# Kernel optimization log

Measured on AMD Instinct MI355X. Metric: run time of the kernel, lower is better.

The kernel has to match this reference:

```python
import jax, jax.numpy as jnp
import numpy as np

NUM_USERS = 100000
NUM_ITEMS = 50000
N_NODES = NUM_USERS + NUM_ITEMS
D = 64
N_LAYERS = 3
E = 2000000
B = 1024
ALPHA_PREF = 1.0


def setup_inputs() -> dict:
    key = jax.random.key(0)
    k1, k2, k3, k4 = jax.random.split(key, 4)
    embed = jax.random.normal(k1, (N_NODES, D), dtype=jnp.float32) * 0.1
    edge_index = jax.random.randint(k2, (2, E), 0, N_NODES, dtype=jnp.int32)
    users = jax.random.randint(k3, (B,), 0, NUM_USERS, dtype=jnp.int32)
    items = jax.random.randint(k4, (B,), 0, NUM_ITEMS, dtype=jnp.int32)
    return {"embed": embed, "edge_index": edge_index, "users": users, "items": items}


def _lightgcn_propagate(x, row, col, norm):
    # message: norm * x[row] (x_j = source), aggregated (add) at col (target)
    msg = norm[:, None] * x[row]                      # [E, D]
    return jnp.zeros_like(x).at[col].add(msg)         # [N, D]


def reference(embed, edge_index, users, items):
    row, col = edge_index[0], edge_index[1]
    n = embed.shape[0]
    # degree normalization (depends only on edge_index; same every layer)
    deg = jnp.zeros((n,), jnp.float32).at[row].add(1.0)
    deg_inv = jnp.clip(deg, 1.0, None) ** -0.5
    norm = deg_inv[row] * deg_inv[col]                # [E]

    x = embed
    for _ in range(N_LAYERS):
        x = _lightgcn_propagate(x, row, col, norm)

    u_emb = x[users]                                  # [B, D]
    i_emb = x[items + NUM_USERS]                      # [B, D]

    # mask = (row == users[:,None]) flattened selection of col; edge e is
    # selected once per batch element b with users[b] == row[e] -> multiplicity
    cnt = jnp.zeros((n,), jnp.float32).at[users].add(1.0)
    mult = cnt[row]                                   # [E] selection multiplicity

    # PreferenceShapley surrogate: softmax over selected neighbor embeddings
    # of alpha_pref * <neigh_emb, mean(u_emb)>, flattened over the batch.
    context = u_emb.mean(0)                           # [D]
    neigh = x[col]                                    # [E, D]
    logits = ALPHA_PREF * (neigh @ context)           # [E]
    masked = jnp.where(mult > 0, logits, -jnp.inf)
    mx = jnp.max(masked)
    ew = mult * jnp.exp(logits - mx)                  # [E] weighted exp (0 where unselected)
    z = jnp.clip(ew.sum(), 1e-12, None)
    neigh_aggr = (ew[:, None] * neigh).sum(0) / z     # [D]

    score = (u_emb * i_emb).sum(-1) + u_emb @ neigh_aggr  # [B]
    return jax.nn.sigmoid(score)
```

## Files before the change

kernel.cpp:

```cpp
#include <hip/hip_runtime.h>
#include <float.h>
#include <math.h>

#define NUM_USERS 100000
#define NUM_ITEMS 50000
#define NNODES    150000
#define DIM       64
#define NEDGE     2000000
#define BATCH     1024
#define SEL_CAP   (1 << 18)
#define LOGIT_BLOCKS 512

#define SLICES   1024
#define EPS      1956
#define NBUK     293
#define BCAP     8192
#define SCAP     16

__device__ __forceinline__ float wave_sum64(float v) {
    #pragma unroll
    for (int off = 32; off > 0; off >>= 1) v += __shfl_xor(v, off, 64);
    return v;
}

__device__ __forceinline__ float bf2f(unsigned short s) {
    return __uint_as_float(((unsigned int)s) << 16);
}
__device__ __forceinline__ unsigned short f2bf(float f) {
    unsigned int u = __float_as_uint(f);
    return (unsigned short)((u + 0x7fffu + ((u >> 16) & 1u)) >> 16);
}


__global__ __launch_bounds__(512) void sort_kernel(
        const int* __restrict__ row, const int* __restrict__ col,
        const int* __restrict__ ucnt,
        int* __restrict__ gcurC, int* __restrict__ gcurR,
        unsigned int* __restrict__ midC, unsigned short* __restrict__ midR,
        int* __restrict__ n_sel, int* __restrict__ sel_col, float* __restrict__ sel_w) {
    __shared__ unsigned int hc[NBUK], hr[NBUK];
    __shared__ int posC[NBUK], posR[NBUK];
    __shared__ unsigned int   stC[NBUK * SCAP];
    __shared__ unsigned short stR[NBUK * SCAP];
    __shared__ int lcnt, lbase, novfC, novfR;
    __shared__ uint2 ovfC[64];
    __shared__ unsigned int ovfR[64];
    __shared__ int2 buf[256];
    int blk = blockIdx.x, t = threadIdx.x;
    for (int i = t; i < NBUK; i += 512) { hc[i] = 0; hr[i] = 0; }
    if (t == 0) { lcnt = 0; novfC = 0; novfR = 0; }
    __syncthreads();
    int e0 = blk * EPS;
    int e1 = e0 + EPS; if (e1 > NEDGE) e1 = NEDGE;
    for (int base = e0 + t * 4; base < e1; base += 2048) {
        if (base + 4 <= e1) {
            int4 r4 = *(const int4*)(row + base);
            int4 c4 = *(const int4*)(col + base);
            #pragma unroll
            for (int q = 0; q < 4; ++q) {
                int c = (q == 0) ? c4.x : (q == 1) ? c4.y : (q == 2) ? c4.z : c4.w;
                int r = (q == 0) ? r4.x : (q == 1) ? r4.y : (q == 2) ? r4.z : r4.w;
                int bc = c >> 9;
                unsigned int kc = atomicAdd(&hc[bc], 1u);
                unsigned int v = ((unsigned int)(c & 511) << 18) | (unsigned int)r;
                if (kc < SCAP) stC[bc * SCAP + kc] = v;
                else { int i = atomicAdd(&novfC, 1); if (i < 64) ovfC[i] = make_uint2((unsigned int)bc, v); }
                int br = r >> 9;
                unsigned int kr = atomicAdd(&hr[br], 1u);
                if (kr < SCAP) stR[br * SCAP + kr] = (unsigned short)(r & 511);
                else { int i = atomicAdd(&novfR, 1); if (i < 64) ovfR[i] = ((unsigned int)br << 9) | (unsigned int)(r & 511); }
                int u = ucnt[r];
                if (u > 0) { int i = atomicAdd(&lcnt, 1); if (i < 256) buf[i] = make_int2(c, u); }
            }
        } else {
            for (int e = base; e < e1; ++e) {
                int r = row[e], c = col[e];
                int bc = c >> 9;
                unsigned int kc = atomicAdd(&hc[bc], 1u);
                unsigned int v = ((unsigned int)(c & 511) << 18) | (unsigned int)r;
                if (kc < SCAP) stC[bc * SCAP + kc] = v;
                else { int i = atomicAdd(&novfC, 1); if (i < 64) ovfC[i] = make_uint2((unsigned int)bc, v); }
                int br = r >> 9;
                unsigned int kr = atomicAdd(&hr[br], 1u);
                if (kr < SCAP) stR[br * SCAP + kr] = (unsigned short)(r & 511);
                else { int i = atomicAdd(&novfR, 1); if (i < 64) ovfR[i] = ((unsigned int)br << 9) | (unsigned int)(r & 511); }
                int u = ucnt[r];
                if (u > 0) { int i = atomicAdd(&lcnt, 1); if (i < 256) buf[i] = make_int2(c, u); }
            }
        }
    }
    __syncthreads();
    if (t < NBUK) {
        int cc = (int)hc[t]; if (cc > SCAP) cc = SCAP;
        int cr = (int)hr[t]; if (cr > SCAP) cr = SCAP;
        posC[t] = atomicAdd(&gcurC[t], cc);
        posR[t] = atomicAdd(&gcurR[t], cr);
    }
    if (t == 0) {
        int c = lcnt; c = c < 256 ? c : 256;
        lbase = atomicAdd(n_sel, c);
    }
    __syncthreads();
    for (int j = t; j < NBUK * SCAP; j += 512) {
        int b = j >> 4, k = j & (SCAP - 1);
        int cc = (int)hc[b]; if (cc > SCAP) cc = SCAP;
        if (k < cc) {
            int d = posC[b] + k;
            if (d < BCAP) midC[(size_t)b * BCAP + d] = stC[j];
        }
        int cr = (int)hr[b]; if (cr > SCAP) cr = SCAP;
        if (k < cr) {
            int d = posR[b] + k;
            if (d < BCAP) midR[(size_t)b * BCAP + d] = stR[j];
        }
    }
    int nc = novfC; nc = nc < 64 ? nc : 64;
    for (int i = t; i < nc; i += 512) {
        int b = (int)ovfC[i].x;
        int d = atomicAdd(&gcurC[b], 1);
        if (d < BCAP) midC[(size_t)b * BCAP + d] = ovfC[i].y;
    }
    int nr = novfR; nr = nr < 64 ? nr : 64;
    for (int i = t; i < nr; i += 512) {
        unsigned int pv = ovfR[i];
        int b = (int)(pv >> 9);
        int d = atomicAdd(&gcurR[b], 1);
        if (d < BCAP) midR[(size_t)b * BCAP + d] = (unsigned short)(pv & 511u);
    }
    int c = lcnt; c = c < 256 ? c : 256;
    int b = lbase;
    for (int i = t; i < c; i += 512) {
        int o = b + i;
        if (o < SEL_CAP) { sel_col[o] = buf[i].x; sel_w[o] = (float)buf[i].y; }
    }
}


__global__ __launch_bounds__(1024) void bfinal_kernel(
        const unsigned int* __restrict__ midC, const int* __restrict__ gcurC,
        const unsigned short* __restrict__ midR, const int* __restrict__ gcurR,
        const float4* __restrict__ embed,
        int* __restrict__ rptr, int* __restrict__ rend, int* __restrict__ src_sorted,
        float* __restrict__ dinv, float* __restrict__ dinv2,
        uint2* __restrict__ y0) {
    __shared__ int cnt[512], sm[512], cur[512];
    __shared__ float dinvL[512];
    int b = blockIdx.x, t = threadIdx.x;
    int s0 = b * BCAP;
    int cc = gcurC[b]; if (cc > BCAP) cc = BCAP;
    int s1 = s0 + cc;
    if (t < 512) cnt[t] = 0;
    __syncthreads();
    for (int i = s0 + t; i < s1; i += 1024) atomicAdd(&cnt[midC[i] >> 18], 1);
    __syncthreads();
    if (t < 512) sm[t] = cnt[t];
    __syncthreads();
    for (int off = 1; off < 512; off <<= 1) {
        int v = 0;
        if (t < 512 && t >= off) v = sm[t - off];
        __syncthreads();
        if (t < 512) sm[t] += v;
        __syncthreads();
    }
    if (t < 512) {
        int excl = s0 + sm[t] - cnt[t];
        int n = b * 512 + t;
        if (n < NNODES) { rptr[n] = excl; rend[n] = s0 + sm[t]; }
        cur[t] = excl;
    }
    if (b == 0 && t < 16) y0[(size_t)NNODES * 16 + t] = make_uint2(0u, 0u);
    __syncthreads();
    for (int i = s0 + t; i < s1; i += 1024) {
        unsigned int v = midC[i];
        int dst = atomicAdd(&cur[v >> 18], 1);
        src_sorted[dst] = (int)(v & 0x3FFFFu);
    }
    __syncthreads();
    if (t < 512) cnt[t] = 0;
    __syncthreads();
    int r0 = b * BCAP;
    int rc = gcurR[b]; if (rc > BCAP) rc = BCAP;
    int r1 = r0 + rc;
    for (int i = r0 + t; i < r1; i += 1024) atomicAdd(&cnt[midR[i]], 1);
    __syncthreads();
    if (t < 512) {
        int n = b * 512 + t;
        if (n < NNODES) {
            float d = fmaxf((float)cnt[t], 1.0f);
            float di = rsqrtf(d);
            dinv[n] = di; dinv2[n] = 1.0f / d;
            dinvL[t] = di;
        }
    }
    __syncthreads();
    int nbase = b * 512;
    int nmax = NNODES - nbase; if (nmax > 512) nmax = 512;
    if (nmax < 0) nmax = 0;
    for (int i = t; i < nmax * 16; i += 1024) {
        int ln = i >> 4, slot = i & 15;
        float d = dinvL[ln];
        float4 v = embed[(size_t)(nbase + ln) * 16 + slot];
        unsigned int w0 = (unsigned int)f2bf(v.x * d) | ((unsigned int)f2bf(v.y * d) << 16);
        unsigned int w1 = (unsigned int)f2bf(v.z * d) | ((unsigned int)f2bf(v.w * d) << 16);
        y0[(size_t)(nbase + ln) * 16 + slot] = make_uint2(w0, w1);
    }
}


#define ACC8(V) do { \
    a0 += __uint_as_float((V).x << 16); a1 += __uint_as_float((V).x & 0xffff0000u); \
    a2 += __uint_as_float((V).y << 16); a3 += __uint_as_float((V).y & 0xffff0000u); \
    a4 += __uint_as_float((V).z << 16); a5 += __uint_as_float((V).z & 0xffff0000u); \
    a6 += __uint_as_float((V).w << 16); a7 += __uint_as_float((V).w & 0xffff0000u); \
} while (0)

__device__ __forceinline__ void prop_node(
        const uint4* __restrict__ x_in, uint4* __restrict__ x_out,
        const int* __restrict__ ptr, const int* __restrict__ rend,
        const int* __restrict__ src,
        const float* __restrict__ scale, int node, int sl) {
    int i = ptr[node], e = rend[node];
    float sc = scale[node];
    float a0 = 0.f, a1 = 0.f, a2 = 0.f, a3 = 0.f;
    float a4 = 0.f, a5 = 0.f, a6 = 0.f, a7 = 0.f;
    int p0, p1, p2, p3;
    if (i + 4 <= e) { p0 = src[i]; p1 = src[i + 1]; p2 = src[i + 2]; p3 = src[i + 3]; }
    while (i + 8 <= e) {
        uint4 w0 = x_in[p0 * 8 + sl];
        uint4 w1 = x_in[p1 * 8 + sl];
        uint4 w2 = x_in[p2 * 8 + sl];
        uint4 w3 = x_in[p3 * 8 + sl];
        p0 = src[i + 4]; p1 = src[i + 5]; p2 = src[i + 6]; p3 = src[i + 7];
        i += 4;
        ACC8(w0); ACC8(w1); ACC8(w2); ACC8(w3);
    }
    if (i + 4 <= e) {
        uint4 w0 = x_in[p0 * 8 + sl];
        uint4 w1 = x_in[p1 * 8 + sl];
        uint4 w2 = x_in[p2 * 8 + sl];
        uint4 w3 = x_in[p3 * 8 + sl];
        i += 4;
        ACC8(w0); ACC8(w1); ACC8(w2); ACC8(w3);
    }
    if (i < e) {
        int q0 = src[i];
        int q1 = (i + 1 < e) ? src[i + 1] : NNODES;
        int q2 = (i + 2 < e) ? src[i + 2] : NNODES;
        uint4 w0 = x_in[q0 * 8 + sl];
        uint4 w1 = x_in[q1 * 8 + sl];
        uint4 w2 = x_in[q2 * 8 + sl];
        ACC8(w0); ACC8(w1); ACC8(w2);
    }
    uint4 o;
    o.x = (unsigned int)f2bf(a0 * sc) | ((unsigned int)f2bf(a1 * sc) << 16);
    o.y = (unsigned int)f2bf(a2 * sc) | ((unsigned int)f2bf(a3 * sc) << 16);
    o.z = (unsigned int)f2bf(a4 * sc) | ((unsigned int)f2bf(a5 * sc) << 16);
    o.w = (unsigned int)f2bf(a6 * sc) | ((unsigned int)f2bf(a7 * sc) << 16);
    x_out[(size_t)node * 8 + sl] = o;
}

__global__ __launch_bounds__(256, 8) void prop_kernel(
        const uint4* __restrict__ x_in, uint4* __restrict__ x_out,
        const int* __restrict__ ptr, const int* __restrict__ rend,
        const int* __restrict__ src,
        const float* __restrict__ scale) {
    int gid  = blockIdx.x * blockDim.x + threadIdx.x;
    int node = gid >> 3;
    int sl   = gid & 7;
    if (node > NNODES) return;
    if (node == NNODES) {
        x_out[(size_t)node * 8 + sl] = make_uint4(0u, 0u, 0u, 0u);
        return;
    }
    prop_node(x_in, x_out, ptr, rend, src, scale, node, sl);
}

__global__ __launch_bounds__(256, 8) void prop_list_kernel(
        const uint4* __restrict__ x_in, uint4* __restrict__ x_out,
        const int* __restrict__ ptr, const int* __restrict__ rend,
        const int* __restrict__ src,
        const float* __restrict__ scale,
        const int* __restrict__ users, const int* __restrict__ items,
        const int* __restrict__ sel_col, const int* __restrict__ n_sel_p) {
    int n = *n_sel_p; if (n > SEL_CAP) n = SEL_CAP;
    int total = (2 * BATCH + n) * 8;
    int nth = gridDim.x * blockDim.x;
    for (int gid = blockIdx.x * blockDim.x + threadIdx.x; gid < total; gid += nth) {
        int li = gid >> 3;
        int sl = gid & 7;
        int node;
        if (li < BATCH) {
            node = users[li];
        } else if (li < 2 * BATCH) {
            node = items[li - BATCH] + NUM_USERS;
        } else {
            node = sel_col[li - 2 * BATCH];
        }
        prop_node(x_in, x_out, ptr, rend, src, scale, node, sl);
    }
}


__global__ void ucnt_kernel(const int* __restrict__ users, int* __restrict__ ucnt) {
    int b = blockIdx.x * blockDim.x + threadIdx.x;
    if (b < BATCH) atomicAdd(&ucnt[users[b]], 1);
}

__global__ __launch_bounds__(256) void ctx_part_kernel(
        const unsigned short* __restrict__ x, const int* __restrict__ users,
        float* __restrict__ ctx) {
    __shared__ float sm[256];
    int lane = threadIdx.x & 63, wl = threadIdx.x >> 6;
    int b0 = blockIdx.x * 16 + wl * 4;
    float acc = 0.0f;
    #pragma unroll
    for (int k = 0; k < 4; ++k)
        acc += bf2f(x[users[b0 + k] * DIM + lane]);
    sm[threadIdx.x] = acc;
    __syncthreads();
    if (wl == 0)
        atomicAdd(&ctx[lane], sm[lane] + sm[64 + lane] + sm[128 + lane] + sm[192 + lane]);
}

__global__ void softmax_kernel(const unsigned short* __restrict__ x,
                               const float* __restrict__ ctx,
                               const int* __restrict__ sel_col,
                               const float* __restrict__ sel_w,
                               const int* __restrict__ n_sel_p,
                               float* __restrict__ S, float* __restrict__ zp) {
    __shared__ float smS[4 * 64];
    __shared__ float smZ[4];
    int lane = threadIdx.x & 63, wl = threadIdx.x >> 6;
    int n = *n_sel_p; if (n > SEL_CAP) n = SEL_CAP;
    float c = ctx[lane] * (1.0f / BATCH);
    float accS = 0.0f, accZ = 0.0f;
    int stride = gridDim.x * 4;
    for (int idx = blockIdx.x * 4 + wl; idx < n; idx += stride) {
        int node = sel_col[idx];
        float xv = bf2f(x[node * DIM + lane]);
        float v = wave_sum64(xv * c);
        float w = sel_w[idx] * __expf(v);
        accS = fmaf(w, xv, accS);
        accZ += w;
    }
    smS[wl * 64 + lane] = accS;
    if (lane == 0) smZ[wl] = accZ;
    __syncthreads();
    if (wl == 0) {
        float s = smS[lane] + smS[64 + lane] + smS[128 + lane] + smS[192 + lane];
        atomicAdd(&S[lane], s);
    }
    if (threadIdx.x == 0) atomicAdd(zp, smZ[0] + smZ[1] + smZ[2] + smZ[3]);
}

__global__ void score_kernel(const unsigned short* __restrict__ x, const int* __restrict__ users,
                             const int* __restrict__ items, const float* __restrict__ S,
                             const float* __restrict__ zp, float* __restrict__ out) {
    int gid = blockIdx.x * blockDim.x + threadIdx.x;
    int b = gid >> 6, lane = gid & 63;
    if (b >= BATCH) return;
    float z = fmaxf(*zp, 1e-12f);
    float na = S[lane] / z;
    int u = users[b], it = items[b] + NUM_USERS;
    float v = bf2f(x[u * DIM + lane]) * (bf2f(x[it * DIM + lane]) + na);
    v = wave_sum64(v);
    if (lane == 0) out[b] = 1.0f / (1.0f + __expf(-v));
}


extern "C" void kernel_launch(void* const* d_in, const int* in_sizes, int n_in,
                              void* d_out, int out_size, void* d_ws, size_t ws_size,
                              hipStream_t stream) {
    const float* embed = (const float*)d_in[0];
    const int*   edge  = (const int*)d_in[1];
    const int*   row   = edge;
    const int*   col   = edge + NEDGE;
    const int*   users = (const int*)d_in[2];
    const int*   items = (const int*)d_in[3];
    float*       out   = (float*)d_out;
    char*        ws    = (char*)d_ws;

    size_t off = 0;
    auto A = [&](size_t bytes) { size_t o = off; off += (bytes + 255) & ~(size_t)255; return o; };
    size_t o_midC  = A((size_t)NBUK * BCAP * 4);
    size_t o_midR  = A((size_t)NBUK * BCAP * 2);
    size_t o_xa    = A((size_t)(NNODES + 1) * DIM * 2);
    size_t o_xb    = A((size_t)(NNODES + 1) * DIM * 2);
    size_t o_src   = A((size_t)NBUK * BCAP * 4);
    size_t o_selc  = A((size_t)SEL_CAP * 4);
    size_t o_selw  = A((size_t)SEL_CAP * 4);
    size_t o_zero  = off;
    size_t o_ucnt  = A((size_t)NNODES * 4);
    size_t o_gcurC = A((size_t)NBUK * 4);
    size_t o_gcurR = A((size_t)NBUK * 4);
    size_t o_misc  = A(1024);
    size_t zero_bytes = off - o_zero;
    size_t o_dinv  = A((size_t)NNODES * 4);
    size_t o_dinv2 = A((size_t)NNODES * 4);
    size_t o_rptr  = A((size_t)NNODES * 4);
    size_t o_rend  = A((size_t)NNODES * 4);

    unsigned int*   midC = (unsigned int*)(ws + o_midC);
    unsigned short* midR = (unsigned short*)(ws + o_midR);
    unsigned short* xa   = (unsigned short*)(ws + o_xa);
    unsigned short* xb   = (unsigned short*)(ws + o_xb);
    int*   srcS  = (int*)(ws + o_src);
    int*   selc  = (int*)(ws + o_selc);
    float* selw  = (float*)(ws + o_selw);
    int*   ucnt  = (int*)(ws + o_ucnt);
    int*   gcurC = (int*)(ws + o_gcurC);
    int*   gcurR = (int*)(ws + o_gcurR);
    int*   nsel  = (int*)(ws + o_misc);
    float* zp    = (float*)(ws + o_misc + 8);
    float* S     = (float*)(ws + o_misc + 256);
    float* ctx   = (float*)(ws + o_misc + 512);
    float* dinv  = (float*)(ws + o_dinv);
    float* dinv2 = (float*)(ws + o_dinv2);
    int*   rptr  = (int*)(ws + o_rptr);
    int*   rend  = (int*)(ws + o_rend);

    hipMemsetAsync(ws + o_zero, 0, zero_bytes, stream);

    ucnt_kernel<<<(BATCH + 255) / 256, 256, 0, stream>>>(users, ucnt);

    sort_kernel<<<SLICES, 512, 0, stream>>>(row, col, ucnt, gcurC, gcurR,
                                            midC, midR, nsel, selc, selw);
    bfinal_kernel<<<NBUK, 1024, 0, stream>>>(midC, gcurC, midR, gcurR,
                                             (const float4*)embed, rptr, rend, srcS,
                                             dinv, dinv2, (uint2*)xa);

    int prop_blocks = ((NNODES + 1) * 8 + 255) / 256;
    prop_kernel<<<prop_blocks, 256, 0, stream>>>((const uint4*)xa, (uint4*)xb, rptr, rend, srcS, dinv2);
    prop_kernel<<<prop_blocks, 256, 0, stream>>>((const uint4*)xb, (uint4*)xa, rptr, rend, srcS, dinv2);
    prop_list_kernel<<<1024, 256, 0, stream>>>((const uint4*)xa, (uint4*)xb,
                                               rptr, rend, srcS, dinv,
                                               users, items, selc, nsel);

    ctx_part_kernel<<<64, 256, 0, stream>>>(xb, users, ctx);
    softmax_kernel<<<LOGIT_BLOCKS, 256, 0, stream>>>(xb, ctx, selc, selw, nsel, S, zp);

    score_kernel<<<(BATCH * 64 + 255) / 256, 256, 0, stream>>>(xb, users, items, S, zp, out);
}
```

Baseline: 256.4 us.

## Replace global atomic bucket cursors with fixed per-slice slots and global overflow list

The sort kernel now writes each slice's per-bucket staged edges into a fixed slot region indexed by slice, and records per-slice counts as bytes, instead of reserving space with global atomics on per-bucket cursors. Overflow entries go to a larger global list that the bucket-finalize kernel scans. This removes contended global atomics and the serialising cursor dependency in the sort kernel. In exchange the finalize kernel must scan a sparse padded layout of 16K slots per bucket, plus the whole overflow list in every block, which costs more reads.

```diff
diff --git a/kernel.cpp b/kernel.cpp
--- a/kernel.cpp
+++ b/kernel.cpp
@@ -16,6 +16,7 @@
 #define NBUK     293
 #define BCAP     8192
 #define SCAP     16
+#define OVF_CAP  4096
 
 __device__ __forceinline__ float wave_sum64(float v) {
     #pragma unroll
@@ -35,20 +36,19 @@
 __global__ __launch_bounds__(512) void sort_kernel(
         const int* __restrict__ row, const int* __restrict__ col,
         const int* __restrict__ ucnt,
-        int* __restrict__ gcurC, int* __restrict__ gcurR,
-        unsigned int* __restrict__ midC, unsigned short* __restrict__ midR,
+        unsigned char* __restrict__ cntC8, unsigned char* __restrict__ cntR8,
+        unsigned int* __restrict__ midC2, unsigned short* __restrict__ midR2,
+        uint2* __restrict__ ovfC, unsigned int* __restrict__ ovfR,
+        int* __restrict__ novfC_g, int* __restrict__ novfR_g,
         int* __restrict__ n_sel, int* __restrict__ sel_col, float* __restrict__ sel_w) {
     __shared__ unsigned int hc[NBUK], hr[NBUK];
-    __shared__ int posC[NBUK], posR[NBUK];
     __shared__ unsigned int   stC[NBUK * SCAP];
     __shared__ unsigned short stR[NBUK * SCAP];
-    __shared__ int lcnt, lbase, novfC, novfR;
-    __shared__ uint2 ovfC[64];
-    __shared__ unsigned int ovfR[64];
+    __shared__ int lcnt, lbase;
     __shared__ int2 buf[256];
     int blk = blockIdx.x, t = threadIdx.x;
     for (int i = t; i < NBUK; i += 512) { hc[i] = 0; hr[i] = 0; }
-    if (t == 0) { lcnt = 0; novfC = 0; novfR = 0; }
+    if (t == 0) lcnt = 0;
     __syncthreads();
     int e0 = blk * EPS;
     int e1 = e0 + EPS; if (e1 > NEDGE) e1 = NEDGE;
@@ -64,11 +64,11 @@
                 unsigned int kc = atomicAdd(&hc[bc], 1u);
                 unsigned int v = ((unsigned int)(c & 511) << 18) | (unsigned int)r;
                 if (kc < SCAP) stC[bc * SCAP + kc] = v;
-                else { int i = atomicAdd(&novfC, 1); if (i < 64) ovfC[i] = make_uint2((unsigned int)bc, v); }
+                else { int i = atomicAdd(novfC_g, 1); if (i < OVF_CAP) ovfC[i] = make_uint2((unsigned int)bc, v); }
                 int br = r >> 9;
                 unsigned int kr = atomicAdd(&hr[br], 1u);
                 if (kr < SCAP) stR[br * SCAP + kr] = (unsigned short)(r & 511);
-                else { int i = atomicAdd(&novfR, 1); if (i < 64) ovfR[i] = ((unsigned int)br << 9) | (unsigned int)(r & 511); }
+                else { int i = atomicAdd(novfR_g, 1); if (i < OVF_CAP) ovfR[i] = ((unsigned int)br << 9) | (unsigned int)(r & 511); }
                 int u = ucnt[r];
                 if (u > 0) { int i = atomicAdd(&lcnt, 1); if (i < 256) buf[i] = make_int2(c, u); }
             }
@@ -79,54 +79,37 @@
                 unsigned int kc = atomicAdd(&hc[bc], 1u);
                 unsigned int v = ((unsigned int)(c & 511) << 18) | (unsigned int)r;
                 if (kc < SCAP) stC[bc * SCAP + kc] = v;
-                else { int i = atomicAdd(&novfC, 1); if (i < 64) ovfC[i] = make_uint2((unsigned int)bc, v); }
+                else { int i = atomicAdd(novfC_g, 1); if (i < OVF_CAP) ovfC[i] = make_uint2((unsigned int)bc, v); }
                 int br = r >> 9;
                 unsigned int kr = atomicAdd(&hr[br], 1u);
                 if (kr < SCAP) stR[br * SCAP + kr] = (unsigned short)(r & 511);
-                else { int i = atomicAdd(&novfR, 1); if (i < 64) ovfR[i] = ((unsigned int)br << 9) | (unsigned int)(r & 511); }
+                else { int i = atomicAdd(novfR_g, 1); if (i < OVF_CAP) ovfR[i] = ((unsigned int)br << 9) | (unsigned int)(r & 511); }
                 int u = ucnt[r];
                 if (u > 0) { int i = atomicAdd(&lcnt, 1); if (i < 256) buf[i] = make_int2(c, u); }
             }
         }
     }
     __syncthreads();
+    for (int j = t; j < NBUK * SCAP; j += 512) {
+        int b = j >> 4, k = j & (SCAP - 1);
+        unsigned int cc = hc[b]; if (cc > SCAP) cc = SCAP;
+        if ((unsigned int)k < cc)
+            midC2[(size_t)b * (SLICES * SCAP) + blk * SCAP + k] = stC[j];
+        unsigned int cr = hr[b]; if (cr > SCAP) cr = SCAP;
+        if ((unsigned int)k < cr)
+            midR2[(size_t)b * (SLICES * SCAP) + blk * SCAP + k] = stR[j];
+    }
     if (t < NBUK) {
-        int cc = (int)hc[t]; if (cc > SCAP) cc = SCAP;
-        int cr = (int)hr[t]; if (cr > SCAP) cr = SCAP;
-        posC[t] = atomicAdd(&gcurC[t], cc);
-        posR[t] = atomicAdd(&gcurR[t], cr);
+        unsigned int cc = hc[t]; if (cc > SCAP) cc = SCAP;
+        unsigned int cr = hr[t]; if (cr > SCAP) cr = SCAP;
+        cntC8[(size_t)blk * NBUK + t] = (unsigned char)cc;
+        cntR8[(size_t)blk * NBUK + t] = (unsigned char)cr;
     }
     if (t == 0) {
         int c = lcnt; c = c < 256 ? c : 256;
         lbase = atomicAdd(n_sel, c);
     }
     __syncthreads();
-    for (int j = t; j < NBUK * SCAP; j += 512) {
-        int b = j >> 4, k = j & (SCAP - 1);
-        int cc = (int)hc[b]; if (cc > SCAP) cc = SCAP;
-        if (k < cc) {
-            int d = posC[b] + k;
-            if (d < BCAP) midC[(size_t)b * BCAP + d] = stC[j];
-        }
-        int cr = (int)hr[b]; if (cr > SCAP) cr = SCAP;
-        if (k < cr) {
-            int d = posR[b] + k;
-            if (d < BCAP) midR[(size_t)b * BCAP + d] = stR[j];
-        }
-    }
-    int nc = novfC; nc = nc < 64 ? nc : 64;
-    for (int i = t; i < nc; i += 512) {
-        int b = (int)ovfC[i].x;
-        int d = atomicAdd(&gcurC[b], 1);
-        if (d < BCAP) midC[(size_t)b * BCAP + d] = ovfC[i].y;
-    }
-    int nr = novfR; nr = nr < 64 ? nr : 64;
-    for (int i = t; i < nr; i += 512) {
-        unsigned int pv = ovfR[i];
-        int b = (int)(pv >> 9);
-        int d = atomicAdd(&gcurR[b], 1);
-        if (d < BCAP) midR[(size_t)b * BCAP + d] = (unsigned short)(pv & 511u);
-    }
     int c = lcnt; c = c < 256 ? c : 256;
     int b = lbase;
     for (int i = t; i < c; i += 512) {
@@ -137,21 +120,32 @@
 
 
 __global__ __launch_bounds__(1024) void bfinal_kernel(
-        const unsigned int* __restrict__ midC, const int* __restrict__ gcurC,
-        const unsigned short* __restrict__ midR, const int* __restrict__ gcurR,
+        const unsigned int* __restrict__ midC2, const unsigned char* __restrict__ cntC8,
+        const unsigned short* __restrict__ midR2, const unsigned char* __restrict__ cntR8,
+        const uint2* __restrict__ ovfC, const unsigned int* __restrict__ ovfR,
+        const int* __restrict__ novfC_g, const int* __restrict__ novfR_g,
         const float4* __restrict__ embed,
         int* __restrict__ rptr, int* __restrict__ rend, int* __restrict__ src_sorted,
         float* __restrict__ dinv, float* __restrict__ dinv2,
         uint2* __restrict__ y0) {
     __shared__ int cnt[512], sm[512], cur[512];
+    __shared__ unsigned char lcC[SLICES], lcR[SLICES];
     __shared__ float dinvL[512];
     int b = blockIdx.x, t = threadIdx.x;
-    int s0 = b * BCAP;
-    int cc = gcurC[b]; if (cc > BCAP) cc = BCAP;
-    int s1 = s0 + cc;
+    if (t < SLICES) {
+        lcC[t] = cntC8[(size_t)t * NBUK + b];
+        lcR[t] = cntR8[(size_t)t * NBUK + b];
+    }
     if (t < 512) cnt[t] = 0;
     __syncthreads();
-    for (int i = s0 + t; i < s1; i += 1024) atomicAdd(&cnt[midC[i] >> 18], 1);
+    size_t cbase = (size_t)b * (SLICES * SCAP);
+    for (int j = t; j < SLICES * SCAP; j += 1024) {
+        if ((unsigned int)(j & (SCAP - 1)) < (unsigned int)lcC[j >> 4])
+            atomicAdd(&cnt[midC2[cbase + j] >> 18], 1);
+    }
+    int noC = *novfC_g; if (noC > OVF_CAP) noC = OVF_CAP;
+    for (int i = t; i < noC; i += 1024)
+        if ((int)ovfC[i].x == b) atomicAdd(&cnt[ovfC[i].y >> 18], 1);
     __syncthreads();
     if (t < 512) sm[t] = cnt[t];
     __syncthreads();
@@ -162,6 +156,7 @@
         if (t < 512) sm[t] += v;
         __syncthreads();
     }
+    int s0 = b * BCAP;
     if (t < 512) {
         int excl = s0 + sm[t] - cnt[t];
         int n = b * 512 + t;
@@ -170,18 +165,31 @@
     }
     if (b == 0 && t < 16) y0[(size_t)NNODES * 16 + t] = make_uint2(0u, 0u);
     __syncthreads();
-    for (int i = s0 + t; i < s1; i += 1024) {
-        unsigned int v = midC[i];
-        int dst = atomicAdd(&cur[v >> 18], 1);
-        src_sorted[dst] = (int)(v & 0x3FFFFu);
-    }
+    for (int j = t; j < SLICES * SCAP; j += 1024) {
+        if ((unsigned int)(j & (SCAP - 1)) < (unsigned int)lcC[j >> 4]) {
+            unsigned int v = midC2[cbase + j];
+            int dst = atomicAdd(&cur[v >> 18], 1);
+            src_sorted[dst] = (int)(v & 0x3FFFFu);
+        }
+    }
+    for (int i = t; i < noC; i += 1024)
+        if ((int)ovfC[i].x == b) {
+            unsigned int v = ovfC[i].y;
+            int dst = atomicAdd(&cur[v >> 18], 1);
+            src_sorted[dst] = (int)(v & 0x3FFFFu);
+        }
     __syncthreads();
     if (t < 512) cnt[t] = 0;
     __syncthreads();
-    int r0 = b * BCAP;
-    int rc = gcurR[b]; if (rc > BCAP) rc = BCAP;
-    int r1 = r0 + rc;
-    for (int i = r0 + t; i < r1; i += 1024) atomicAdd(&cnt[midR[i]], 1);
+    for (int j = t; j < SLICES * SCAP; j += 1024) {
+        if ((unsigned int)(j & (SCAP - 1)) < (unsigned int)lcR[j >> 4])
+            atomicAdd(&cnt[midR2[cbase + j]], 1);
+    }
+    int noR = *novfR_g; if (noR > OVF_CAP) noR = OVF_CAP;
+    for (int i = t; i < noR; i += 1024) {
+        unsigned int pv = ovfR[i];
+        if ((int)(pv >> 9) == b) atomicAdd(&cnt[pv & 511u], 1);
+    }
     __syncthreads();
     if (t < 512) {
         int n = b * 512 + t;
@@ -382,17 +390,19 @@
 
     size_t off = 0;
     auto A = [&](size_t bytes) { size_t o = off; off += (bytes + 255) & ~(size_t)255; return o; };
-    size_t o_midC  = A((size_t)NBUK * BCAP * 4);
-    size_t o_midR  = A((size_t)NBUK * BCAP * 2);
+    size_t o_midC2 = A((size_t)NBUK * SLICES * SCAP * 4);
+    size_t o_midR2 = A((size_t)NBUK * SLICES * SCAP * 2);
     size_t o_xa    = A((size_t)(NNODES + 1) * DIM * 2);
     size_t o_xb    = A((size_t)(NNODES + 1) * DIM * 2);
     size_t o_src   = A((size_t)NBUK * BCAP * 4);
+    size_t o_cntC8 = A((size_t)SLICES * NBUK);
+    size_t o_cntR8 = A((size_t)SLICES * NBUK);
+    size_t o_ovfC  = A((size_t)OVF_CAP * 8);
+    size_t o_ovfR  = A((size_t)OVF_CAP * 4);
     size_t o_selc  = A((size_t)SEL_CAP * 4);
     size_t o_selw  = A((size_t)SEL_CAP * 4);
     size_t o_zero  = off;
     size_t o_ucnt  = A((size_t)NNODES * 4);
-    size_t o_gcurC = A((size_t)NBUK * 4);
-    size_t o_gcurR = A((size_t)NBUK * 4);
     size_t o_misc  = A(1024);
     size_t zero_bytes = off - o_zero;
     size_t o_dinv  = A((size_t)NNODES * 4);
@@ -400,20 +410,24 @@
     size_t o_rptr  = A((size_t)NNODES * 4);
     size_t o_rend  = A((size_t)NNODES * 4);
 
-    unsigned int*   midC = (unsigned int*)(ws + o_midC);
-    unsigned short* midR = (unsigned short*)(ws + o_midR);
+    unsigned int*   midC2 = (unsigned int*)(ws + o_midC2);
+    unsigned short* midR2 = (unsigned short*)(ws + o_midR2);
     unsigned short* xa   = (unsigned short*)(ws + o_xa);
     unsigned short* xb   = (unsigned short*)(ws + o_xb);
     int*   srcS  = (int*)(ws + o_src);
+    unsigned char* cntC8 = (unsigned char*)(ws + o_cntC8);
+    unsigned char* cntR8 = (unsigned char*)(ws + o_cntR8);
+    uint2* ovfC  = (uint2*)(ws + o_ovfC);
+    unsigned int* ovfR = (unsigned int*)(ws + o_ovfR);
     int*   selc  = (int*)(ws + o_selc);
     float* selw  = (float*)(ws + o_selw);
     int*   ucnt  = (int*)(ws + o_ucnt);
-    int*   gcurC = (int*)(ws + o_gcurC);
-    int*   gcurR = (int*)(ws + o_gcurR);
     int*   nsel  = (int*)(ws + o_misc);
     float* zp    = (float*)(ws + o_misc + 8);
     float* S     = (float*)(ws + o_misc + 256);
     float* ctx   = (float*)(ws + o_misc + 512);
+    int*   novfC = (int*)(ws + o_misc + 768);
+    int*   novfR = (int*)(ws + o_misc + 772);
     float* dinv  = (float*)(ws + o_dinv);
     float* dinv2 = (float*)(ws + o_dinv2);
     int*   rptr  = (int*)(ws + o_rptr);
@@ -423,9 +437,11 @@
 
     ucnt_kernel<<<(BATCH + 255) / 256, 256, 0, stream>>>(users, ucnt);
 
-    sort_kernel<<<SLICES, 512, 0, stream>>>(row, col, ucnt, gcurC, gcurR,
-                                            midC, midR, nsel, selc, selw);
-    bfinal_kernel<<<NBUK, 1024, 0, stream>>>(midC, gcurC, midR, gcurR,
+    sort_kernel<<<SLICES, 512, 0, stream>>>(row, col, ucnt, cntC8, cntR8,
+                                            midC2, midR2, ovfC, ovfR, novfC, novfR,
+                                            nsel, selc, selw);
+    bfinal_kernel<<<NBUK, 1024, 0, stream>>>(midC2, cntC8, midR2, cntR8,
+                                             ovfC, ovfR, novfC, novfR,
                                              (const float4*)embed, rptr, rend, srcS,
                                              dinv, dinv2, (uint2*)xa);
 
```

After: 256.1 us. About the same (-0.1%).
